# Kernel tuning notes

Measured on AMD Instinct MI355X. Metric: run time of the kernel, lower is better.

Reference implementation:

```python
import math
import jax, jax.numpy as jnp
import numpy as np

V, D, H, L, F, T, B = 32000, 1024, 16, 4, 4096, 1024, 2
HD = D // H
EPS = 1e-5


def make_pe(max_len, d):
    pos = np.arange(max_len)[:, None].astype(np.float32)
    div = np.exp(np.arange(0, d, 2).astype(np.float32) * (-math.log(10000.0) / d))
    pe = np.zeros((max_len, d), dtype=np.float32)
    pe[:, 0::2] = np.sin(pos * div)
    pe[:, 1::2] = np.cos(pos * div)
    return jnp.asarray(pe)


def setup_inputs() -> dict:
    key = jax.random.key(0)
    ks = jax.random.split(key, 12)
    s = 0.02
    inp = {
        'tokens': jax.random.randint(ks[0], (B, T), 0, V, dtype=jnp.int32),
        'mask': jnp.tril(jnp.ones((T, T), dtype=jnp.int32)),
        'emb': jax.random.normal(ks[1], (V, D), jnp.float32) * s,
        'pe': make_pe(T, D),
        'ln1_g': jnp.ones((L, D)), 'ln1_b': jnp.zeros((L, D)),
        'Wqkv': jax.random.normal(ks[2], (L, D, 3 * D), jnp.float32) * s,
        'bqkv': jnp.zeros((L, 3 * D)),
        'Wproj': jax.random.normal(ks[3], (L, D, D), jnp.float32) * s,
        'bproj': jnp.zeros((L, D)),
        'ln2_g': jnp.ones((L, D)), 'ln2_b': jnp.zeros((L, D)),
        'W1': jax.random.normal(ks[4], (L, D, F), jnp.float32) * s,
        'b1': jnp.zeros((L, F)),
        'W2': jax.random.normal(ks[5], (L, F, D), jnp.float32) * s,
        'b2': jnp.zeros((L, D)),
        'lnf_g': jnp.ones((D,)), 'lnf_b': jnp.zeros((D,)),
        'out_b': jnp.zeros((V,)),
    }
    return inp


def layer_norm(x, g, b):
    m = jnp.mean(x, axis=-1, keepdims=True)
    v = jnp.mean((x - m) ** 2, axis=-1, keepdims=True)
    return (x - m) / jnp.sqrt(v + EPS) * g + b


def attention(x, mask, Wqkv, bqkv, Wproj, bproj):
    b, t, c = x.shape
    qkv = (x @ Wqkv + bqkv).reshape(b, t, 3, H, HD)
    q, k, v = jnp.moveaxis(qkv, 2, 0)  # each [B,T,H,HD]
    q = q.transpose(0, 2, 1, 3)  # [B,H,T,HD]
    k = k.transpose(0, 2, 1, 3)
    v = v.transpose(0, 2, 1, 3)
    scores = jnp.einsum('bhqd,bhkd->bhqk', q, k) / math.sqrt(HD)
    scores = jnp.where(mask[None, None] == 0, -1e9, scores)
    attn = jax.nn.softmax(scores, axis=-1)
    out = jnp.einsum('bhqk,bhkd->bhqd', attn, v)
    out = out.transpose(0, 2, 1, 3).reshape(b, t, c)
    return out @ Wproj + bproj, attn


def reference(tokens, mask, emb, pe, ln1_g, ln1_b, Wqkv, bqkv, Wproj, bproj,
              ln2_g, ln2_b, W1, b1, W2, b2, lnf_g, lnf_b, out_b):
    x = emb[tokens] + pe[:tokens.shape[1]]
    attn = None
    for i in range(L):
        a, attn = attention(layer_norm(x, ln1_g[i], ln1_b[i]), mask,
                            Wqkv[i], bqkv[i], Wproj[i], bproj[i])
        x = x + a
        h = layer_norm(x, ln2_g[i], ln2_b[i])
        h = jax.nn.gelu(h @ W1[i] + b1[i], approximate=False) @ W2[i] + b2[i]
        x = x + h
    x = layer_norm(x, lnf_g, lnf_b)
    logits = x @ emb.T + out_b  # weight tying
    return logits, attn
```

## Files before the change

### kernel.cpp

```cpp
#include <hip/hip_runtime.h>
#include <cstdint>

#define DEV static __device__ __forceinline__

typedef unsigned short u16;
typedef __bf16 bf16x8 __attribute__((ext_vector_type(8)));
typedef float f32x4 __attribute__((ext_vector_type(4)));
typedef unsigned short u16x4 __attribute__((ext_vector_type(4)));

constexpr int V = 32000, D = 1024, H = 16, L = 4, F = 4096, T = 1024, B = 2;
constexpr int HD = 64;

DEV u16 f2bf(float f) {
    union { float f; uint32_t i; } c; c.f = f;
    uint32_t x = c.i;
    return (u16)((x + 0x7fffu + ((x >> 16) & 1u)) >> 16);
}
DEV bf16x8 ld8(const u16* p) { return *reinterpret_cast<const bf16x8*>(p); }

DEV void gl16(const void* g, void* l) {
    __builtin_amdgcn_global_load_lds((const __attribute__((address_space(1))) void*)g,
                                     (__attribute__((address_space(3))) void*)l, 16, 0, 0);
}

DEV void castT4_dev(int t, int x, int y, u16 (*tl)[33],
        const float* __restrict__ Wqkv, const float* __restrict__ Wproj,
        const float* __restrict__ W1, const float* __restrict__ W2,
        u16* __restrict__ wt) {
    const float* src; u16* dst; int Rr, Cc;
    if (t < 768)       { src = Wqkv;  dst = wt;                       Rr = D; Cc = 3 * D; }
    else if (t < 1024) { src = Wproj; dst = wt + 3 * D * D;           Rr = D; Cc = D; t -= 768; }
    else if (t < 2048) { src = W1;    dst = wt + 4 * D * D;           Rr = D; Cc = F; t -= 1024; }
    else               { src = W2;    dst = wt + 4 * D * D + D * F;   Rr = F; Cc = D; t -= 2048; }
    int colStrips = Cc >> 7;
    int r0 = (t / colStrips) * 32;
    int c0 = (t % colStrips) * 128;
    for (int i = 0; i < 4; i++) {
        int cc = c0 + i * 32;
        __syncthreads();
#pragma unroll
        for (int j = 0; j < 4; j++)
            tl[y + j * 8][x] = f2bf(src[(size_t)(r0 + y + j * 8) * Cc + cc + x]);
        __syncthreads();
#pragma unroll
        for (int j = 0; j < 4; j++)
            dst[(size_t)(cc + y + j * 8) * Rr + r0 + x] = tl[x][y + j * 8];
    }
}

__global__ __launch_bounds__(256) void k_emblnT(const int* __restrict__ tok,
        const float* __restrict__ emb, const float* __restrict__ pe,
        const float* __restrict__ g, const float* __restrict__ b,
        float* __restrict__ x, u16* __restrict__ out,
        const float* __restrict__ Wqkv, const float* __restrict__ Wproj,
        const float* __restrict__ W1, const float* __restrict__ W2,
        u16* __restrict__ wt) {
    __shared__ u16 tl[32][33];
    __shared__ float ps[4], ps2[4];
    int row = blockIdx.x, tid = threadIdx.x;
    if (row >= B * T) {
        castT4_dev(row - B * T, tid & 31, tid >> 5, tl, Wqkv, Wproj, W1, W2, wt);
        return;
    }
    int t = row & (T - 1);
    int vv = tok[row];
    f32x4 v = ((const f32x4*)(emb + (size_t)vv * D))[tid] + ((const f32x4*)(pe + (size_t)t * D))[tid];
    ((f32x4*)(x + (size_t)row * D))[tid] = v;
    float s = v[0] + v[1] + v[2] + v[3];
    float s2 = v[0]*v[0] + v[1]*v[1] + v[2]*v[2] + v[3]*v[3];
#pragma unroll
    for (int m = 1; m < 64; m <<= 1) { s += __shfl_xor(s, m); s2 += __shfl_xor(s2, m); }
    int wave = tid >> 6;
    if ((tid & 63) == 0) { ps[wave] = s; ps2[wave] = s2; }
    __syncthreads();
    s = ps[0] + ps[1] + ps[2] + ps[3];
    s2 = ps2[0] + ps2[1] + ps2[2] + ps2[3];
    float mean = s * (1.f / D);
    float var = s2 * (1.f / D) - mean * mean;
    float r = rsqrtf(var + 1e-5f);
    f32x4 gg = ((const f32x4*)g)[tid];
    f32x4 bb = ((const f32x4*)b)[tid];
    u16x4 o;
#pragma unroll
    for (int j = 0; j < 4; j++) o[j] = f2bf((v[j] - mean) * r * gg[j] + bb[j]);
    ((u16x4*)(out + (size_t)row * D))[tid] = o;
}

template <int S, bool DOCAST>
__global__ __launch_bounds__(256) void k_redlnT(const float* __restrict__ pp,
        const float* __restrict__ bias, float* __restrict__ x,
        const float* __restrict__ g, const float* __restrict__ b,
        u16* __restrict__ out,
        const float* __restrict__ Wqkv, const float* __restrict__ Wproj,
        const float* __restrict__ W1, const float* __restrict__ W2,
        u16* __restrict__ wt) {
    __shared__ u16 tl[32][33];
    __shared__ float ps[4], ps2[4];
    int row = blockIdx.x, tid = threadIdx.x;
    if (DOCAST && row >= B * T) {
        castT4_dev(row - B * T, tid & 31, tid >> 5, tl, Wqkv, Wproj, W1, W2, wt);
        return;
    }
    f32x4 v = ((const f32x4*)(x + (size_t)row * D))[tid];
#pragma unroll
    for (int s = 0; s < S; s++)
        v += ((const f32x4*)(pp + ((size_t)s * (B * T) + row) * D))[tid];
    v += ((const f32x4*)bias)[tid];
    ((f32x4*)(x + (size_t)row * D))[tid] = v;
    float s = v[0] + v[1] + v[2] + v[3];
    float s2 = v[0]*v[0] + v[1]*v[1] + v[2]*v[2] + v[3]*v[3];
#pragma unroll
    for (int m = 1; m < 64; m <<= 1) { s += __shfl_xor(s, m); s2 += __shfl_xor(s2, m); }
    int wave = tid >> 6;
    if ((tid & 63) == 0) { ps[wave] = s; ps2[wave] = s2; }
    __syncthreads();
    s = ps[0] + ps[1] + ps[2] + ps[3];
    s2 = ps2[0] + ps2[1] + ps2[2] + ps2[3];
    float mean = s * (1.f / D);
    float var = s2 * (1.f / D) - mean * mean;
    float r = rsqrtf(var + 1e-5f);
    f32x4 gg = ((const f32x4*)g)[tid];
    f32x4 bb = ((const f32x4*)b)[tid];
    u16x4 o;
#pragma unroll
    for (int j = 0; j < 4; j++) o[j] = f2bf((v[j] - mean) * r * gg[j] + bb[j]);
    ((u16x4*)(out + (size_t)row * D))[tid] = o;
}

__global__ __launch_bounds__(256) void k_cast(const float* __restrict__ src,
        u16* __restrict__ dst) {
    int i = (blockIdx.x * 256 + threadIdx.x) * 4;
    f32x4 v = *(const f32x4*)(src + i);
    u16x4 o;
#pragma unroll
    for (int j = 0; j < 4; j++) o[j] = f2bf(v[j]);
    *(u16x4*)(dst + i) = o;
}

DEV bf16x8 ldf(const u16* half, int row, int lhi) {
    int lb = row * 64 + lhi * 16;
    lb ^= ((lb >> 9) & 1) << 5;
    return *(const bf16x8*)((const char*)half + lb);
}
DEV void stg(const u16* gb, int ld, int kc, u16* dstBase, int wave, int lane) {
#pragma unroll
    for (int i = 0; i < 2; i++) {
        int p = (wave * 2 + i) * 64 + lane;
        int l = p ^ (((p >> 5) & 1) << 1);
        gl16(gb + (size_t)(l >> 2) * ld + kc + (l & 3) * 8, dstBase + (wave * 2 + i) * 512);
    }
}
#define SB_BAR() do { __builtin_amdgcn_sched_barrier(0); __builtin_amdgcn_s_barrier(); } while (0)

template <int EPI, bool VT>
__global__ __launch_bounds__(256, 2) void k_gemm4(
        const u16* __restrict__ A, int lda,
        const u16* __restrict__ Bt, int ldb,
        const float* __restrict__ bias,
        void* __restrict__ Cv, int ldc, int K, u16* __restrict__ vT) {
    __shared__ u16 lds[2][4][128 * 32];
    int gm = gridDim.x, nwg = gm * gridDim.y;
    int orig = blockIdx.y * gm + blockIdx.x;
    int xcd = orig & 7, idx = orig >> 3;
    int q = nwg >> 3, rr = nwg & 7;
    int wg = (xcd < rr ? xcd * (q + 1) : rr * (q + 1) + (xcd - rr) * q) + idx;
    int m0 = (wg % gm) * 128, n0 = (wg / gm) * 128;
    int koff = (EPI == 4) ? blockIdx.z * K : 0;
    int tid = threadIdx.x, wave = tid >> 6, lane = tid & 63;
    int llo = lane & 15, lhi = lane >> 4;
    int wm = wave >> 1, wn = wave & 1;
    const u16* Ab = A + (size_t)m0 * lda;
    const u16* Bb = Bt + (size_t)n0 * ldb;
    int nk = K >> 6;
    f32x4 acc[4][4] = {};
    stg(Ab, lda, koff + 0,   &lds[0][0][0], wave, lane);
    stg(Bb, ldb, koff + 0,   &lds[0][1][0], wave, lane);
    stg(Ab, lda, koff + 32,  &lds[0][2][0], wave, lane);
    stg(Bb, ldb, koff + 32,  &lds[0][3][0], wave, lane);
    stg(Ab, lda, koff + 64,  &lds[1][0][0], wave, lane);
    stg(Bb, ldb, koff + 64,  &lds[1][1][0], wave, lane);
    stg(Ab, lda, koff + 96,  &lds[1][2][0], wave, lane);
    asm volatile("s_waitcnt vmcnt(10)");
    SB_BAR();
    for (int t = 0; t < nk; ++t) {
        const int bf = t & 1;
        bf16x8 af[4], b0, b1;
#pragma unroll
        for (int mi = 0; mi < 4; mi++) af[mi] = ldf(&lds[bf][0][0], wm * 64 + mi * 16 + llo, lhi);
        b0 = ldf(&lds[bf][1][0], wn * 64 + llo, lhi);
        b1 = ldf(&lds[bf][1][0], wn * 64 + 16 + llo, lhi);
        if (t + 1 < nk) stg(Bb, ldb, koff + (t + 1) * 64 + 32, &lds[bf ^ 1][3][0], wave, lane);
        __builtin_amdgcn_s_setprio(1);
#pragma unroll
        for (int mi = 0; mi < 4; mi++) {
            acc[mi][0] = __builtin_amdgcn_mfma_f32_16x16x32_bf16(af[mi], b0, acc[mi][0], 0, 0, 0);
            acc[mi][1] = __builtin_amdgcn_mfma_f32_16x16x32_bf16(af[mi], b1, acc[mi][1], 0, 0, 0);
        }
        __builtin_amdgcn_s_setprio(0);
        SB_BAR();
        b0 = ldf(&lds[bf][1][0], wn * 64 + 32 + llo, lhi);
        b1 = ldf(&lds[bf][1][0], wn * 64 + 48 + llo, lhi);
        if (t + 2 < nk) stg(Ab, lda, koff + (t + 2) * 64, &lds[bf][0][0], wave, lane);
        __builtin_amdgcn_s_setprio(1);
#pragma unroll
        for (int mi = 0; mi < 4; mi++) {
            acc[mi][2] = __builtin_amdgcn_mfma_f32_16x16x32_bf16(af[mi], b0, acc[mi][2], 0, 0, 0);
            acc[mi][3] = __builtin_amdgcn_mfma_f32_16x16x32_bf16(af[mi], b1, acc[mi][3], 0, 0, 0);
        }
        __builtin_amdgcn_s_setprio(0);
        if (t + 2 < nk)      { asm volatile("s_waitcnt vmcnt(10)"); }
        else if (t + 1 < nk) { asm volatile("s_waitcnt vmcnt(8)"); }
        else                 { asm volatile("s_waitcnt vmcnt(0)"); }
        SB_BAR();
#pragma unroll
        for (int mi = 0; mi < 4; mi++) af[mi] = ldf(&lds[bf][2][0], wm * 64 + mi * 16 + llo, lhi);
        b0 = ldf(&lds[bf][3][0], wn * 64 + llo, lhi);
        b1 = ldf(&lds[bf][3][0], wn * 64 + 16 + llo, lhi);
        if (t + 2 < nk) stg(Bb, ldb, koff + (t + 2) * 64, &lds[bf][1][0], wave, lane);
        __builtin_amdgcn_s_setprio(1);
#pragma unroll
        for (int mi = 0; mi < 4; mi++) {
            acc[mi][0] = __builtin_amdgcn_mfma_f32_16x16x32_bf16(af[mi], b0, acc[mi][0], 0, 0, 0);
            acc[mi][1] = __builtin_amdgcn_mfma_f32_16x16x32_bf16(af[mi], b1, acc[mi][1], 0, 0, 0);
        }
        __builtin_amdgcn_s_setprio(0);
        SB_BAR();
        b0 = ldf(&lds[bf][3][0], wn * 64 + 32 + llo, lhi);
        b1 = ldf(&lds[bf][3][0], wn * 64 + 48 + llo, lhi);
        if (t + 2 < nk) stg(Ab, lda, koff + (t + 2) * 64 + 32, &lds[bf][2][0], wave, lane);
        __builtin_amdgcn_s_setprio(1);
#pragma unroll
        for (int mi = 0; mi < 4; mi++) {
            acc[mi][2] = __builtin_amdgcn_mfma_f32_16x16x32_bf16(af[mi], b0, acc[mi][2], 0, 0, 0);
            acc[mi][3] = __builtin_amdgcn_mfma_f32_16x16x32_bf16(af[mi], b1, acc[mi][3], 0, 0, 0);
        }
        __builtin_amdgcn_s_setprio(0);
        if (t + 1 < nk) {
            if (t + 2 < nk) { asm volatile("s_waitcnt vmcnt(10)"); }
            else            { asm volatile("s_waitcnt vmcnt(4)"); }
        }
        SB_BAR();
    }
#pragma unroll
    for (int ni = 0; ni < 4; ni++) {
        int col = n0 + wn * 64 + ni * 16 + llo;
        float bb = 0.f;
        if (EPI != 4) bb = bias[col];
#pragma unroll
        for (int mi = 0; mi < 4; mi++) {
            int row0 = m0 + wm * 64 + mi * 16 + lhi * 4;
            if (VT && col >= 2 * D) {
                int dv = col - 2 * D;
                int b_ = row0 >> 10, t_ = row0 & (T - 1);
                u16x4 pk;
#pragma unroll
                for (int r = 0; r < 4; r++) pk[r] = f2bf(acc[mi][ni][r] + bb);
                *(u16x4*)(vT + ((size_t)(b_ * 16 + (dv >> 6)) * HD + (dv & 63)) * T + t_) = pk;
            } else {
#pragma unroll
                for (int r = 0; r < 4; r++) {
                    int row = row0 + r;
                    float o = acc[mi][ni][r] + bb;
                    if (EPI == 1) o = 0.5f * o * (1.f + erff(o * 0.70710678118f));
                    if (EPI == 4) {
                        ((float*)Cv)[((size_t)blockIdx.z * (B * T) + row) * ldc + col] = o;
                    } else {
                        ((u16*)Cv)[(size_t)row * ldc + col] = f2bf(o);
                    }
                }
            }
        }
    }
}

__global__ __launch_bounds__(512, 2) void k_gemm8(
        const u16* __restrict__ A, int lda,
        const u16* __restrict__ Bt, int ldb,
        const float* __restrict__ bias,
        float* __restrict__ C, int ldc, int K) {
    __shared__ u16 lds[2][4][256 * 32];
    int gm = gridDim.x, nwg = gm * gridDim.y;
    int orig = blockIdx.y * gm + blockIdx.x;
    int xcd = orig & 7, idx = orig >> 3;
    int q = nwg >> 3, rr = nwg & 7;
    int wg = (xcd < rr ? xcd * (q + 1) : rr * (q + 1) + (xcd - rr) * q) + idx;
    int m0 = (wg % gm) * 256, n0 = (wg / gm) * 256;
    int tid = threadIdx.x, wave = tid >> 6, lane = tid & 63;
    int llo = lane & 15, lhi = lane >> 4;
    int wm = wave >> 2, wn = wave & 3;
    const u16* Ab = A + (size_t)m0 * lda;
    const u16* Bb = Bt + (size_t)n0 * ldb;
    int nk = K >> 6;
    f32x4 acc[8][4] = {};
    stg(Ab, lda, 0,   &lds[0][0][0], wave, lane);
    stg(Bb, ldb, 0,   &lds[0][1][0], wave, lane);
    stg(Ab, lda, 32,  &lds[0][2][0], wave, lane);
    stg(Bb, ldb, 32,  &lds[0][3][0], wave, lane);
    stg(Ab, lda, 64,  &lds[1][0][0], wave, lane);
    stg(Bb, ldb, 64,  &lds[1][1][0], wave, lane);
    stg(Ab, lda, 96,  &lds[1][2][0], wave, lane);
    asm volatile("s_waitcnt vmcnt(10)");
    SB_BAR();
    for (int t = 0; t < nk; ++t) {
        const int bf = t & 1;
        bf16x8 af[8], b0, b1;
#pragma unroll
        for (int mi = 0; mi < 8; mi++) af[mi] = ldf(&lds[bf][0][0], wm * 128 + mi * 16 + llo, lhi);
        b0 = ldf(&lds[bf][1][0], wn * 64 + llo, lhi);
        b1 = ldf(&lds[bf][1][0], wn * 64 + 16 + llo, lhi);
        if (t + 1 < nk) stg(Bb, ldb, (t + 1) * 64 + 32, &lds[bf ^ 1][3][0], wave, lane);
        __builtin_amdgcn_s_setprio(1);
#pragma unroll
        for (int mi = 0; mi < 8; mi++) {
            acc[mi][0] = __builtin_amdgcn_mfma_f32_16x16x32_bf16(af[mi], b0, acc[mi][0], 0, 0, 0);
            acc[mi][1] = __builtin_amdgcn_mfma_f32_16x16x32_bf16(af[mi], b1, acc[mi][1], 0, 0, 0);
        }
        __builtin_amdgcn_s_setprio(0);
        SB_BAR();
        b0 = ldf(&lds[bf][1][0], wn * 64 + 32 + llo, lhi);
        b1 = ldf(&lds[bf][1][0], wn * 64 + 48 + llo, lhi);
        if (t + 2 < nk) stg(Ab, lda, (t + 2) * 64, &lds[bf][0][0], wave, lane);
        __builtin_amdgcn_s_setprio(1);
#pragma unroll
        for (int mi = 0; mi < 8; mi++) {
            acc[mi][2] = __builtin_amdgcn_mfma_f32_16x16x32_bf16(af[mi], b0, acc[mi][2], 0, 0, 0);
            acc[mi][3] = __builtin_amdgcn_mfma_f32_16x16x32_bf16(af[mi], b1, acc[mi][3], 0, 0, 0);
        }
        __builtin_amdgcn_s_setprio(0);
        if (t + 2 < nk)      { asm volatile("s_waitcnt vmcnt(10)"); }
        else if (t + 1 < nk) { asm volatile("s_waitcnt vmcnt(8)"); }
        else                 { asm volatile("s_waitcnt vmcnt(0)"); }
        SB_BAR();
#pragma unroll
        for (int mi = 0; mi < 8; mi++) af[mi] = ldf(&lds[bf][2][0], wm * 128 + mi * 16 + llo, lhi);
        b0 = ldf(&lds[bf][3][0], wn * 64 + llo, lhi);
        b1 = ldf(&lds[bf][3][0], wn * 64 + 16 + llo, lhi);
        if (t + 2 < nk) stg(Bb, ldb, (t + 2) * 64, &lds[bf][1][0], wave, lane);
        __builtin_amdgcn_s_setprio(1);
#pragma unroll
        for (int mi = 0; mi < 8; mi++) {
            acc[mi][0] = __builtin_amdgcn_mfma_f32_16x16x32_bf16(af[mi], b0, acc[mi][0], 0, 0, 0);
            acc[mi][1] = __builtin_amdgcn_mfma_f32_16x16x32_bf16(af[mi], b1, acc[mi][1], 0, 0, 0);
        }
        __builtin_amdgcn_s_setprio(0);
        SB_BAR();
        b0 = ldf(&lds[bf][3][0], wn * 64 + 32 + llo, lhi);
        b1 = ldf(&lds[bf][3][0], wn * 64 + 48 + llo, lhi);
        if (t + 2 < nk) stg(Ab, lda, (t + 2) * 64 + 32, &lds[bf][2][0], wave, lane);
        __builtin_amdgcn_s_setprio(1);
#pragma unroll
        for (int mi = 0; mi < 8; mi++) {
            acc[mi][2] = __builtin_amdgcn_mfma_f32_16x16x32_bf16(af[mi], b0, acc[mi][2], 0, 0, 0);
            acc[mi][3] = __builtin_amdgcn_mfma_f32_16x16x32_bf16(af[mi], b1, acc[mi][3], 0, 0, 0);
        }
        __builtin_amdgcn_s_setprio(0);
        if (t + 1 < nk) {
            if (t + 2 < nk) { asm volatile("s_waitcnt vmcnt(10)"); }
            else            { asm volatile("s_waitcnt vmcnt(4)"); }
        }
        SB_BAR();
    }
#pragma unroll
    for (int ni = 0; ni < 4; ni++) {
        int col = n0 + wn * 64 + ni * 16 + llo;
        float bb = bias[col];
#pragma unroll
        for (int mi = 0; mi < 8; mi++) {
            int row0 = m0 + wm * 128 + mi * 16 + lhi * 4;
#pragma unroll
            for (int r = 0; r < 4; r++)
                C[(size_t)(row0 + r) * ldc + col] = acc[mi][ni][r] + bb;
        }
    }
}

template <int PW>
__global__ __launch_bounds__(256) void k_fattn(const u16* __restrict__ qkv,
        const u16* __restrict__ vT, u16* __restrict__ out, float* __restrict__ attnF) {
    __shared__ u16 plds[4][16 * 40];
    int bh = blockIdx.y; int b = bh >> 4, h = bh & 15;
    int tid = threadIdx.x, wave = tid >> 6, lane = tid & 63;
    int llo = lane & 15, lhi = lane >> 4;
    int i0 = blockIdx.x * 64 + wave * 16;
    const u16* qb = qkv + (size_t)b * T * (3 * D) + h * HD;
    const u16* kb = qb + D;
    const u16* vt = vT + (size_t)bh * HD * T;
    bf16x8 q0 = ld8(qb + (size_t)(i0 + llo) * (3 * D) + lhi * 8);
    bf16x8 q1 = ld8(qb + (size_t)(i0 + llo) * (3 * D) + 32 + lhi * 8);
    int qrow = i0 + llo;
    float m = -3e38f, s = 0.f;
    f32x4 oacc[4] = {};
    u16* pw = &plds[wave][0];
    for (int k0 = 0; k0 < i0 + 16; k0 += 32) {
        f32x4 sc0 = {}, sc1 = {};
        {
            bf16x8 kf0 = ld8(kb + (size_t)(k0 + llo) * (3 * D) + lhi * 8);
            bf16x8 kf1 = ld8(kb + (size_t)(k0 + llo) * (3 * D) + 32 + lhi * 8);
            sc0 = __builtin_amdgcn_mfma_f32_16x16x32_bf16(kf0, q0, sc0, 0, 0, 0);
            sc0 = __builtin_amdgcn_mfma_f32_16x16x32_bf16(kf1, q1, sc0, 0, 0, 0);
        }
        if (k0 + 16 < i0 + 16) {
            bf16x8 kf0 = ld8(kb + (size_t)(k0 + 16 + llo) * (3 * D) + lhi * 8);
            bf16x8 kf1 = ld8(kb + (size_t)(k0 + 16 + llo) * (3 * D) + 32 + lhi * 8);
            sc1 = __builtin_amdgcn_mfma_f32_16x16x32_bf16(kf0, q0, sc1, 0, 0, 0);
            sc1 = __builtin_amdgcn_mfma_f32_16x16x32_bf16(kf1, q1, sc1, 0, 0, 0);
        }
        float vv[8]; float mx = m;
#pragma unroll
        for (int hf = 0; hf < 2; hf++)
#pragma unroll
            for (int r = 0; r < 4; r++) {
                int k = k0 + hf * 16 + lhi * 4 + r;
                float x = (hf ? sc1[r] : sc0[r]) * 0.125f;
                float v = (k <= qrow) ? x : -3e38f;
                vv[hf * 4 + r] = v;
                mx = fmaxf(mx, v);
            }
        mx = fmaxf(mx, __shfl_xor(mx, 16));
        mx = fmaxf(mx, __shfl_xor(mx, 32));
        float p[8]; float ps = 0.f;
#pragma unroll
        for (int j = 0; j < 8; j++) { p[j] = __expf(vv[j] - mx); ps += p[j]; }
        ps += __shfl_xor(ps, 16);
        ps += __shfl_xor(ps, 32);
        float scale = __expf(m - mx);
        s = s * scale + ps;
        m = mx;
        float sr[4];
#pragma unroll
        for (int r = 0; r < 4; r++) sr[r] = __shfl(scale, lhi * 4 + r);
#pragma unroll
        for (int n = 0; n < 4; n++)
#pragma unroll
            for (int r = 0; r < 4; r++) oacc[n][r] *= sr[r];
#pragma unroll
        for (int hf = 0; hf < 2; hf++) {
            u16x4 pk;
#pragma unroll
            for (int r = 0; r < 4; r++) pk[r] = f2bf(p[hf * 4 + r]);
            *(u16x4*)(pw + llo * 40 + hf * 16 + lhi * 4) = pk;
        }
        bf16x8 pa = ld8(pw + llo * 40 + lhi * 8);
#pragma unroll
        for (int n = 0; n < 4; n++) {
            bf16x8 vb = ld8(vt + (size_t)(n * 16 + llo) * T + k0 + lhi * 8);
            oacc[n] = __builtin_amdgcn_mfma_f32_16x16x32_bf16(pa, vb, oacc[n], 0, 0, 0);
        }
    }
    float inv = 1.f / s;
    float ir[4];
#pragma unroll
    for (int r = 0; r < 4; r++) ir[r] = __shfl(inv, lhi * 4 + r);
#pragma unroll
    for (int n = 0; n < 4; n++)
#pragma unroll
        for (int r = 0; r < 4; r++) {
            int i = i0 + lhi * 4 + r, c = n * 16 + llo;
            out[(size_t)(b * T + i) * D + h * HD + c] = f2bf(oacc[n][r] * ir[r]);
        }
    if (PW) {
        float* ar = attnF + ((size_t)bh * T + qrow) * T;
        for (int j0 = 0; j0 < T; j0 += 16) {
            f32x4 pv = {};
            if (j0 <= qrow) {
                if (j0 < i0 + 16) {
                    bf16x8 kf0 = ld8(kb + (size_t)(j0 + llo) * (3 * D) + lhi * 8);
                    bf16x8 kf1 = ld8(kb + (size_t)(j0 + llo) * (3 * D) + 32 + lhi * 8);
                    f32x4 sc = {};
                    sc = __builtin_amdgcn_mfma_f32_16x16x32_bf16(kf0, q0, sc, 0, 0, 0);
                    sc = __builtin_amdgcn_mfma_f32_16x16x32_bf16(kf1, q1, sc, 0, 0, 0);
#pragma unroll
                    for (int r = 0; r < 4; r++) {
                        int j = j0 + lhi * 4 + r;
                        pv[r] = (j <= qrow) ? __expf(sc[r] * 0.125f - m) * inv : 0.f;
                    }
                }
            }
            *(f32x4*)(ar + j0 + lhi * 4) = pv;
        }
    }
}

extern "C" void kernel_launch(void* const* d_in, const int* in_sizes, int n_in,
                              void* d_out, int out_size, void* d_ws, size_t ws_size,
                              hipStream_t stream) {
    const int*   tok   = (const int*)d_in[0];
    const float* emb   = (const float*)d_in[2];
    const float* pe    = (const float*)d_in[3];
    const float* ln1g  = (const float*)d_in[4];
    const float* ln1b  = (const float*)d_in[5];
    const float* Wqkv  = (const float*)d_in[6];
    const float* bqkv  = (const float*)d_in[7];
    const float* Wproj = (const float*)d_in[8];
    const float* bproj = (const float*)d_in[9];
    const float* ln2g  = (const float*)d_in[10];
    const float* ln2b  = (const float*)d_in[11];
    const float* W1    = (const float*)d_in[12];
    const float* b1    = (const float*)d_in[13];
    const float* W2    = (const float*)d_in[14];
    const float* b2    = (const float*)d_in[15];
    const float* lnfg  = (const float*)d_in[16];
    const float* lnfb  = (const float*)d_in[17];
    const float* outb  = (const float*)d_in[18];

    float* logits  = (float*)d_out;
    float* attnF   = logits + (size_t)B * T * V;

    char* w = (char*)d_ws;
    float* x    = (float*)w;  w += (size_t)B * T * D * 4;
    u16* lnout  = (u16*)w;    w += (size_t)B * T * D * 2;
    u16* qkv    = (u16*)w;    w += (size_t)B * T * 3 * D * 2;
    u16* vT     = (u16*)w;    w += (size_t)B * H * HD * T * 2;
    u16* aout   = (u16*)w;    w += (size_t)B * T * D * 2;
    char* tail = w;
    u16* hmid   = (u16*)w;    w += (size_t)B * T * F * 2;
    u16* WTL    = (u16*)w;    w += (size_t)(5 * D * D + 2 * D * F) * 2;
    float* pp   = (float*)w;  w += (size_t)4 * B * T * D * 4;
    u16* embB   = (u16*)tail;

    dim3 blk(256);
    const int CG = 3072;
    k_emblnT<<<dim3(B * T + CG), blk, 0, stream>>>(tok, emb, pe, ln1g, ln1b, x, lnout,
        Wqkv, Wproj, W1, W2, WTL);

    for (int l = 0; l < L; l++) {
        k_gemm4<0, true><<<dim3(B * T / 128, 3 * D / 128), blk, 0, stream>>>(
            lnout, D, WTL, D, bqkv + l * 3 * D, qkv, 3 * D, D, vT);
        if (l == L - 1)
            k_fattn<1><<<dim3(T / 64, B * H), blk, 0, stream>>>(qkv, vT, aout, attnF);
        else
            k_fattn<0><<<dim3(T / 64, B * H), blk, 0, stream>>>(qkv, vT, aout, attnF);
        k_gemm4<4, false><<<dim3(B * T / 128, D / 128, 4), blk, 0, stream>>>(
            aout, D, WTL + (size_t)3 * D * D, D, nullptr, pp, D, D / 4, nullptr);
        k_redlnT<4, false><<<dim3(B * T), blk, 0, stream>>>(pp, bproj + l * D, x,
            ln2g + l * D, ln2b + l * D, lnout, nullptr, nullptr, nullptr, nullptr, nullptr);
        k_gemm4<1, false><<<dim3(B * T / 128, F / 128), blk, 0, stream>>>(
            lnout, D, WTL + (size_t)4 * D * D, D, b1 + l * F, hmid, F, D, nullptr);
        k_gemm4<4, false><<<dim3(B * T / 128, D / 128, 4), blk, 0, stream>>>(
            hmid, F, WTL + (size_t)4 * D * D + D * F, F, nullptr, pp, D, F / 4, nullptr);
        if (l < L - 1) {
            k_redlnT<4, true><<<dim3(B * T + CG), blk, 0, stream>>>(pp, b2 + l * D, x,
                ln1g + (l + 1) * D, ln1b + (l + 1) * D, lnout,
                Wqkv + (size_t)(l + 1) * D * 3 * D, Wproj + (size_t)(l + 1) * D * D,
                W1 + (size_t)(l + 1) * D * F, W2 + (size_t)(l + 1) * F * D, WTL);
        } else {
            k_redlnT<4, false><<<dim3(B * T), blk, 0, stream>>>(pp, b2 + l * D, x,
                lnfg, lnfb, lnout, nullptr, nullptr, nullptr, nullptr, nullptr);
        }
    }
    k_cast<<<dim3(V * D / 1024), blk, 0, stream>>>(emb, embB);
    k_gemm8<<<dim3(B * T / 256, V / 256), dim3(512), 0, stream>>>(
        lnout, D, embB, D, outb, logits, V, D);
}
```

Before: 998.4 us.

## Fold embedding bf16 cast into attention kernels across layers

Removes the standalone fp32-to-bf16 cast of the embedding matrix before the logits GEMM. Each layer's attention launch gets 500 extra blocks that each convert a 16K-element slice, so the cast is spread over four layers and overlaps with attention work. The attention grid is flattened to 1D to make room for these blocks. The bf16 embedding copy now needs its own workspace region, since it can no longer share the tail buffer that hmid and the weights reuse.

```diff
diff --git a/kernel.cpp b/kernel.cpp
--- a/kernel.cpp
+++ b/kernel.cpp
@@ -125,16 +125,6 @@
 #pragma unroll
     for (int j = 0; j < 4; j++) o[j] = f2bf((v[j] - mean) * r * gg[j] + bb[j]);
     ((u16x4*)(out + (size_t)row * D))[tid] = o;
-}
-
-__global__ __launch_bounds__(256) void k_cast(const float* __restrict__ src,
-        u16* __restrict__ dst) {
-    int i = (blockIdx.x * 256 + threadIdx.x) * 4;
-    f32x4 v = *(const f32x4*)(src + i);
-    u16x4 o;
-#pragma unroll
-    for (int j = 0; j < 4; j++) o[j] = f2bf(v[j]);
-    *(u16x4*)(dst + i) = o;
 }
 
 DEV bf16x8 ldf(const u16* half, int row, int lhi) {
@@ -376,12 +366,28 @@
 
 template <int PW>
 __global__ __launch_bounds__(256) void k_fattn(const u16* __restrict__ qkv,
-        const u16* __restrict__ vT, u16* __restrict__ out, float* __restrict__ attnF) {
+        const u16* __restrict__ vT, u16* __restrict__ out, float* __restrict__ attnF,
+        const float* __restrict__ embf, u16* __restrict__ embB, int castBase) {
     __shared__ u16 plds[4][16 * 40];
-    int bh = blockIdx.y; int b = bh >> 4, h = bh & 15;
-    int tid = threadIdx.x, wave = tid >> 6, lane = tid & 63;
+    int gid = blockIdx.x, tid = threadIdx.x;
+    if (gid >= 512) {
+        size_t base = ((size_t)castBase + (gid - 512)) * 16384;
+        const f32x4* src = (const f32x4*)(embf + base);
+        u16x4* dst = (u16x4*)(embB + base);
+#pragma unroll 4
+        for (int i = 0; i < 16; i++) {
+            f32x4 v = src[i * 256 + tid];
+            u16x4 o;
+#pragma unroll
+            for (int j = 0; j < 4; j++) o[j] = f2bf(v[j]);
+            dst[i * 256 + tid] = o;
+        }
+        return;
+    }
+    int bh = gid >> 4; int b = bh >> 4, h = bh & 15;
+    int wave = tid >> 6, lane = tid & 63;
     int llo = lane & 15, lhi = lane >> 4;
-    int i0 = blockIdx.x * 64 + wave * 16;
+    int i0 = (gid & 15) * 64 + wave * 16;
     const u16* qb = qkv + (size_t)b * T * (3 * D) + h * HD;
     const u16* kb = qb + D;
     const u16* vt = vT + (size_t)bh * HD * T;
@@ -512,14 +518,14 @@
     u16* qkv    = (u16*)w;    w += (size_t)B * T * 3 * D * 2;
     u16* vT     = (u16*)w;    w += (size_t)B * H * HD * T * 2;
     u16* aout   = (u16*)w;    w += (size_t)B * T * D * 2;
-    char* tail = w;
     u16* hmid   = (u16*)w;    w += (size_t)B * T * F * 2;
     u16* WTL    = (u16*)w;    w += (size_t)(5 * D * D + 2 * D * F) * 2;
     float* pp   = (float*)w;  w += (size_t)4 * B * T * D * 4;
-    u16* embB   = (u16*)tail;
+    u16* embB   = (u16*)w;    w += (size_t)V * D * 2;
 
     dim3 blk(256);
     const int CG = 3072;
+    const int CC = 500;
     k_emblnT<<<dim3(B * T + CG), blk, 0, stream>>>(tok, emb, pe, ln1g, ln1b, x, lnout,
         Wqkv, Wproj, W1, W2, WTL);
 
@@ -527,9 +533,11 @@
         k_gemm4<0, true><<<dim3(B * T / 128, 3 * D / 128), blk, 0, stream>>>(
             lnout, D, WTL, D, bqkv + l * 3 * D, qkv, 3 * D, D, vT);
         if (l == L - 1)
-            k_fattn<1><<<dim3(T / 64, B * H), blk, 0, stream>>>(qkv, vT, aout, attnF);
+            k_fattn<1><<<dim3(512 + CC), blk, 0, stream>>>(qkv, vT, aout, attnF,
+                emb, embB, l * CC);
         else
-            k_fattn<0><<<dim3(T / 64, B * H), blk, 0, stream>>>(qkv, vT, aout, attnF);
+            k_fattn<0><<<dim3(512 + CC), blk, 0, stream>>>(qkv, vT, aout, attnF,
+                emb, embB, l * CC);
         k_gemm4<4, false><<<dim3(B * T / 128, D / 128, 4), blk, 0, stream>>>(
             aout, D, WTL + (size_t)3 * D * D, D, nullptr, pp, D, D / 4, nullptr);
         k_redlnT<4, false><<<dim3(B * T), blk, 0, stream>>>(pp, bproj + l * D, x,
@@ -548,7 +556,6 @@
                 lnfg, lnfb, lnout, nullptr, nullptr, nullptr, nullptr, nullptr);
         }
     }
-    k_cast<<<dim3(V * D / 1024), blk, 0, stream>>>(emb, embB);
     k_gemm8<<<dim3(B * T / 256, V / 256), dim3(512), 0, stream>>>(
         lnout, D, embB, D, outb, logits, V, D);
 }
```

Measured after the change: 986.4 us. No clear change (-1.2%).
